# Kernel optimization log

Hardware: AMD Instinct MI355X
Metric: run time of the kernel (lower is better)

## Reference

```python
import jax, jax.numpy as jnp
import numpy as np

DROP_BLOCK = 7  # matches init_kwargs drop_block


def setup_inputs() -> dict:
    key = jax.random.key(0)
    k1, k2 = jax.random.split(key)
    x = jax.random.normal(k1, (32, 512, 56, 56), dtype=jnp.float32)
    T = jax.random.randint(k2, (32, 512, 1, 1), 0, 2, dtype=jnp.int32)
    return {"x": x, "T": T}


def _local_mask(x, T):
    B, C, H, W = x.shape
    xf = x.reshape(-1, H, W)                      # [B*C, H, W]
    marked = (T.reshape(-1) > 0)                  # [B*C] bool; which channels get a cutout
    # Argmax location per channel (original uses h for both div and mod)
    idx = jnp.argmax(xf.reshape(xf.shape[0], -1), axis=1)  # [B*C]
    mi = idx // H
    mj = idx % H
    half = DROP_BLOCK // 2  # floor(drop_block / 2)
    h1 = jnp.clip(mi - half, 0, H - 1)
    h2 = jnp.clip(mi + half, 0, H - 1)
    w1 = jnp.clip(mj - half, 0, W - 1)
    w2 = jnp.clip(mj + half, 0, W - 1)
    rows = jnp.arange(H)[None, :, None]           # [1, H, 1]
    cols = jnp.arange(W)[None, None, :]           # [1, 1, W]
    # S[i, h1:h2, w1:w2] = 0 (exclusive upper bound, as in torch slicing)
    in_box = ((rows >= h1[:, None, None]) & (rows < h2[:, None, None]) &
              (cols >= w1[:, None, None]) & (cols < w2[:, None, None]))
    S = jnp.where(in_box, 0.0, 1.0).astype(xf.dtype)       # [B*C, H, W]
    lam = (H * W) / S.sum(axis=(1, 2))                      # [B*C]
    masked = xf * S * lam[:, None, None]
    out = jnp.where(marked[:, None, None], masked, xf)
    return out.reshape(B, C, H, W)


def reference(x, T):
    return _local_mask(x, T)
```

## Files before the change

### kernel.cpp

```cpp
#include <hip/hip_runtime.h>

#define HH 56
#define WW 56
#define HW 3136
#define NV4 784
#define BLK 256

typedef float f4 __attribute__((ext_vector_type(4)));

__global__ __launch_bounds__(BLK) void local_mask_kernel(
    const float* __restrict__ x, const int* __restrict__ T, float* __restrict__ out)
{
    const int ch  = blockIdx.x;
    const int tid = threadIdx.x;

    const bool marked = (T[ch] > 0);

    const f4* __restrict__ xin  = (const f4*)(x   + (size_t)ch * HW);
    f4* __restrict__       xout = (f4*)      (out + (size_t)ch * HW);

    f4 v[4];
    #pragma unroll
    for (int k = 0; k < 4; ++k) {
        int i = tid + k * BLK;
        if (i < NV4) v[k] = __builtin_nontemporal_load(&xin[i]);
    }

    if (!marked) {
        #pragma unroll
        for (int k = 0; k < 4; ++k) {
            int i = tid + k * BLK;
            if (i < NV4) __builtin_nontemporal_store(v[k], &xout[i]);
        }
        return;
    }

    float bestv = -__builtin_inff();
    int   besti = 0;
    #pragma unroll
    for (int k = 0; k < 4; ++k) {
        int i = tid + k * BLK;
        if (i < NV4) {
            const f4 f = v[k];
            const int base = i * 4;
            if (f.x > bestv) { bestv = f.x; besti = base;     }
            if (f.y > bestv) { bestv = f.y; besti = base + 1; }
            if (f.z > bestv) { bestv = f.z; besti = base + 2; }
            if (f.w > bestv) { bestv = f.w; besti = base + 3; }
        }
    }

    #pragma unroll
    for (int off = 32; off > 0; off >>= 1) {
        float ov = __shfl_down(bestv, (unsigned)off);
        int   oi = __shfl_down(besti, (unsigned)off);
        if (ov > bestv || (ov == bestv && oi < besti)) { bestv = ov; besti = oi; }
    }

    __shared__ float s_v[4];
    __shared__ int   s_i[4];

    const int wave = tid >> 6;
    const int lane = tid & 63;
    if (lane == 0) { s_v[wave] = bestv; s_i[wave] = besti; }
    __syncthreads();

    float bv = s_v[0]; int bi = s_i[0];
    #pragma unroll
    for (int w = 1; w < 4; ++w) {
        const float wv = s_v[w]; const int wi = s_i[w];
        if (wv > bv || (wv == bv && wi < bi)) { bv = wv; bi = wi; }
    }

    const int mi = bi / HH;
    const int mj = bi - mi * HH;
    const int h1 = max(mi - 3, 0);
    const int h2 = min(mi + 3, HH - 1);
    const int w1 = max(mj - 3, 0);
    const int w2 = min(mj + 3, WW - 1);
    const int zeros = (h2 - h1) * (w2 - w1);
    const float lam = (float)HW / (float)(HW - zeros);

    #pragma unroll
    for (int k = 0; k < 4; ++k) {
        int i = tid + k * BLK;
        if (i < NV4) {
            const f4  f    = v[k];
            const int row  = i / 14;
            const int col0 = (i - row * 14) * 4;
            const bool rin = (row >= h1) & (row < h2);
            f4 o;
            o.x = (rin & (col0     >= w1) & (col0     < w2)) ? 0.0f : f.x * lam;
            o.y = (rin & (col0 + 1 >= w1) & (col0 + 1 < w2)) ? 0.0f : f.y * lam;
            o.z = (rin & (col0 + 2 >= w1) & (col0 + 2 < w2)) ? 0.0f : f.z * lam;
            o.w = (rin & (col0 + 3 >= w1) & (col0 + 3 < w2)) ? 0.0f : f.w * lam;
            __builtin_nontemporal_store(o, &xout[i]);
        }
    }
}

extern "C" void kernel_launch(void* const* d_in, const int* in_sizes, int n_in,
                              void* d_out, int out_size, void* d_ws, size_t ws_size,
                              hipStream_t stream) {
    const float* x = (const float*)d_in[0];
    const int*   T = (const int*)d_in[1];
    float*     out = (float*)d_out;
    const int channels = in_sizes[0] / HW;
    local_mask_kernel<<<channels, BLK, 0, stream>>>(x, T, out);
}
```

Before: 323.9 us.

## Assign one wavefront per channel to drop shared-memory block reduction

Each wavefront now processes an entire channel, and a block covers four channels. The argmax reduction finishes with wave shuffles alone, so the shared-memory exchange and __syncthreads are gone. In exchange each thread holds 13 float4 values in registers, and each wave issues more loads in sequence, which raises register pressure and may lower occupancy.

```diff
diff --git a/kernel.cpp b/kernel.cpp
--- a/kernel.cpp
+++ b/kernel.cpp
@@ -5,43 +5,48 @@
 #define HW 3136
 #define NV4 784
 #define BLK 256
+#define CPB 4
 
 typedef float f4 __attribute__((ext_vector_type(4)));
 
 __global__ __launch_bounds__(BLK) void local_mask_kernel(
-    const float* __restrict__ x, const int* __restrict__ T, float* __restrict__ out)
+    const float* __restrict__ x, const int* __restrict__ T, float* __restrict__ out,
+    int channels)
 {
-    const int ch  = blockIdx.x;
-    const int tid = threadIdx.x;
+    const int wave = threadIdx.x >> 6;
+    const int lane = threadIdx.x & 63;
+    const int ch   = blockIdx.x * CPB + wave;
+    if (ch >= channels) return;
 
     const bool marked = (T[ch] > 0);
 
     const f4* __restrict__ xin  = (const f4*)(x   + (size_t)ch * HW);
     f4* __restrict__       xout = (f4*)      (out + (size_t)ch * HW);
 
-    f4 v[4];
+    const bool tail = (lane < 16);
+    f4 v[13];
     #pragma unroll
-    for (int k = 0; k < 4; ++k) {
-        int i = tid + k * BLK;
-        if (i < NV4) v[k] = __builtin_nontemporal_load(&xin[i]);
-    }
+    for (int k = 0; k < 12; ++k)
+        v[k] = __builtin_nontemporal_load(&xin[lane + k * 64]);
+    if (tail)
+        v[12] = __builtin_nontemporal_load(&xin[lane + 768]);
 
     if (!marked) {
         #pragma unroll
-        for (int k = 0; k < 4; ++k) {
-            int i = tid + k * BLK;
-            if (i < NV4) __builtin_nontemporal_store(v[k], &xout[i]);
-        }
+        for (int k = 0; k < 12; ++k)
+            __builtin_nontemporal_store(v[k], &xout[lane + k * 64]);
+        if (tail)
+            __builtin_nontemporal_store(v[12], &xout[lane + 768]);
         return;
     }
 
     float bestv = -__builtin_inff();
     int   besti = 0;
     #pragma unroll
-    for (int k = 0; k < 4; ++k) {
-        int i = tid + k * BLK;
-        if (i < NV4) {
-            const f4 f = v[k];
+    for (int k = 0; k < 13; ++k) {
+        if (k < 12 || tail) {
+            const int i    = lane + k * 64;
+            const f4  f    = v[k];
             const int base = i * 4;
             if (f.x > bestv) { bestv = f.x; besti = base;     }
             if (f.y > bestv) { bestv = f.y; besti = base + 1; }
@@ -56,21 +61,7 @@
         int   oi = __shfl_down(besti, (unsigned)off);
         if (ov > bestv || (ov == bestv && oi < besti)) { bestv = ov; besti = oi; }
     }
-
-    __shared__ float s_v[4];
-    __shared__ int   s_i[4];
-
-    const int wave = tid >> 6;
-    const int lane = tid & 63;
-    if (lane == 0) { s_v[wave] = bestv; s_i[wave] = besti; }
-    __syncthreads();
-
-    float bv = s_v[0]; int bi = s_i[0];
-    #pragma unroll
-    for (int w = 1; w < 4; ++w) {
-        const float wv = s_v[w]; const int wi = s_i[w];
-        if (wv > bv || (wv == bv && wi < bi)) { bv = wv; bi = wi; }
-    }
+    const int bi = __shfl(besti, 0);
 
     const int mi = bi / HH;
     const int mj = bi - mi * HH;
@@ -82,9 +73,9 @@
     const float lam = (float)HW / (float)(HW - zeros);
 
     #pragma unroll
-    for (int k = 0; k < 4; ++k) {
-        int i = tid + k * BLK;
-        if (i < NV4) {
+    for (int k = 0; k < 13; ++k) {
+        if (k < 12 || tail) {
+            const int i    = lane + k * 64;
             const f4  f    = v[k];
             const int row  = i / 14;
             const int col0 = (i - row * 14) * 4;
@@ -106,5 +97,6 @@
     const int*   T = (const int*)d_in[1];
     float*     out = (float*)d_out;
     const int channels = in_sizes[0] / HW;
-    local_mask_kernel<<<channels, BLK, 0, stream>>>(x, T, out);
+    const int blocks = (channels + CPB - 1) / CPB;
+    local_mask_kernel<<<blocks, BLK, 0, stream>>>(x, T, out, channels);
 }
```

Measured after the change: 328.0 us. No clear change (+1.3%).
